# Kernel tuning notes

Measured on AMD Instinct MI355X. Metric: run time of the kernel, lower is better.

Reference implementation:

```python
import jax, jax.numpy as jnp
import numpy as np


def _gcn_conv(x, W, b, src, dst, num_nodes):
    # x: [N, F_in], W: [F_in, F_out], b: [F_out]
    # src/dst already include self-loops. Symmetric normalization per PyG GCNConv.
    ones = jnp.ones(src.shape[0], dtype=x.dtype)
    deg = jax.ops.segment_sum(ones, dst, num_segments=num_nodes)  # in-degree w/ self-loops
    dinv = jnp.where(deg > 0, jax.lax.rsqrt(deg), 0.0)
    norm = dinv[src] * dinv[dst]                                  # [E]
    h = x @ W                                                     # [N, F_out]
    msg = h[src] * norm[:, None]                                  # gather + scale
    out = jax.ops.segment_sum(msg, dst, num_segments=num_nodes)   # scatter-add
    return out + b


def setup_inputs() -> dict:
    key = jax.random.key(0)
    k1, k2, k3, k4, k5, k6 = jax.random.split(key, 6)
    N, E = 1000000, 4000000
    x = jax.random.normal(k1, (N, 4), dtype=jnp.float32)
    edge_index = jax.random.randint(k2, (2, E), 0, N, dtype=jnp.int64)
    W1 = jax.random.normal(k3, (4, 16), dtype=jnp.float32) * 0.5
    b1 = jax.random.normal(k4, (16,), dtype=jnp.float32) * 0.1
    W2 = jax.random.normal(k5, (16, 2), dtype=jnp.float32) * 0.25
    b2 = jax.random.normal(k6, (2,), dtype=jnp.float32) * 0.1
    return {"x": x, "edge_index": edge_index, "num_nodes": N,
            "W1": W1, "b1": b1, "W2": W2, "b2": b2}


def reference(x, edge_index, num_nodes, W1, b1, W2, b2):
    # Add self-loops once (GCNConv default add_self_loops=True)
    loop = jnp.arange(num_nodes, dtype=edge_index.dtype)
    src = jnp.concatenate([edge_index[0], loop])
    dst = jnp.concatenate([edge_index[1], loop])
    h = jax.nn.relu(_gcn_conv(x, W1, b1, src, dst, num_nodes))
    h = _gcn_conv(h, W2, b2, src, dst, num_nodes)
    return jax.nn.log_softmax(h, axis=1)
```

## Files before the change

kernel.cpp:

```cpp
#include <hip/hip_runtime.h>


typedef unsigned int u32;

#define BSHIFT 11
#define BNODES 2048
#define MAXBINS 1024
#define EPB 16384

__device__ __forceinline__ u32 pack_bf16(float a, float b) {
    u32 ua = __float_as_uint(a), ub = __float_as_uint(b);
    ua += 0x7FFFu + ((ua >> 16) & 1u);
    ub += 0x7FFFu + ((ub >> 16) & 1u);
    return (ua >> 16) | (ub & 0xFFFF0000u);
}
__device__ __forceinline__ float bf_lo(u32 p) { return __uint_as_float(p << 16); }
__device__ __forceinline__ float bf_hi(u32 p) { return __uint_as_float(p & 0xFFFF0000u); }

__global__ void k_bincount(const int* __restrict__ src, const int* __restrict__ dst,
                           int E, int NBINS, u32 HALF,
                           u32* __restrict__ binTotal, u32* __restrict__ bh) {
    __shared__ u32 h[MAXBINS];
    const int tid = threadIdx.x;
    for (int j = tid; j < MAXBINS; j += 256) h[j] = 0;
    __syncthreads();
    const int start = blockIdx.x * EPB;
    const int end = min(start + EPB, E);
    for (int e = start + tid; e < end; e += 256) {
        u32 d = (u32)dst[e];
        u32 b = ((d >> BSHIFT) << 1) | ((u32)src[e] >= HALF ? 1u : 0u);
        atomicAdd(&h[b], 1u);
    }
    __syncthreads();
    u32* bhrow = bh + (size_t)blockIdx.x * MAXBINS;
    for (int j = tid; j < NBINS; j += 256) {
        u32 c = h[j];
        bhrow[j] = c;
        if (c) atomicAdd(&binTotal[j], c);
    }
}

__global__ void k_binscan(const u32* __restrict__ binTotal,
                          u32* __restrict__ binBase,
                          u32* __restrict__ cursor, int NBINS, int E) {
    __shared__ u32 s[MAXBINS];
    const int tid = threadIdx.x;
    u32 v = (tid < NBINS) ? binTotal[tid] : 0u;
    s[tid] = v;
    __syncthreads();
    for (int d = 1; d < MAXBINS; d <<= 1) {
        u32 t = (tid >= d) ? s[tid - d] : 0u;
        __syncthreads();
        s[tid] += t;
        __syncthreads();
    }
    u32 excl = s[tid] - v;
    if (tid < NBINS) { binBase[tid] = excl; cursor[tid] = excl; }
    if (tid == 0) binBase[NBINS] = (u32)E;
}

__global__ void k_binscatter(const int* __restrict__ src, const int* __restrict__ dst,
                             int E, int NBINS, u32 HALF, u32* __restrict__ cursor,
                             const u32* __restrict__ bh, u32* __restrict__ rec) {
    __shared__ u32 h[MAXBINS];
    const int tid = threadIdx.x;
    const u32* bhrow = bh + (size_t)blockIdx.x * MAXBINS;
    for (int j = tid; j < MAXBINS; j += 256) h[j] = 0;
    __syncthreads();
    for (int j = tid; j < NBINS; j += 256) {
        u32 c = bhrow[j];
        if (c) h[j] = atomicAdd(&cursor[j], c);
    }
    __syncthreads();
    const int start = blockIdx.x * EPB;
    const int end = min(start + EPB, E);
    for (int e = start + tid; e < end; e += 256) {
        u32 d = (u32)dst[e];
        u32 sv = (u32)src[e];
        u32 b = ((d >> BSHIFT) << 1) | (sv >= HALF ? 1u : 0u);
        u32 slot = atomicAdd(&h[b], 1u);
        rec[slot] = sv | ((d & (BNODES - 1u)) << 20);
    }
}

__global__ void k_deg(const u32* __restrict__ rec, const u32* __restrict__ binBase,
                      const float4* __restrict__ x,
                      float* __restrict__ dinv, uint2* __restrict__ xd, int N) {
    __shared__ u32 deg[BNODES];
    const int tid = threadIdx.x;
    const int b = blockIdx.x;
    for (int j = tid; j < BNODES; j += 512) deg[j] = 0;
    __syncthreads();
    const u32 s0 = binBase[2 * b], s1 = binBase[2 * b + 2];
    for (u32 i = s0 + tid; i < s1; i += 512)
        atomicAdd(&deg[rec[i] >> 20], 1u);
    __syncthreads();
    const int nodeBase = b << BSHIFT;
    for (int n = tid; n < BNODES; n += 512) {
        int gn = nodeBase + n;
        if (gn < N) {
            float d = rsqrtf((float)(deg[n] + 1u));
            dinv[gn] = d;
            float4 xi = x[gn];
            xd[gn] = make_uint2(pack_bf16(xi.x * d, xi.y * d),
                                pack_bf16(xi.z * d, xi.w * d));
        }
    }
}

__global__ void k_l1(const u32* __restrict__ rec, const u32* __restrict__ binBase,
                     const float* __restrict__ dinv, const uint2* __restrict__ xd,
                     const float* __restrict__ W1, const float* __restrict__ b1,
                     const float* __restrict__ W2,
                     u32* __restrict__ h2, int N) {
    __shared__ float agg[BNODES * 4];
    const int tid = threadIdx.x;
    const int b = blockIdx.x;
    for (int j = tid; j < BNODES * 4; j += 1024) agg[j] = 0.f;
    __syncthreads();
    const u32 s0 = binBase[2 * b], s1 = binBase[2 * b + 2];

#define L1_EDGE(I) do {                                   \
        u32 r = rec[I];                                   \
        u32 s = r & 0xFFFFFu;                             \
        float* p = &agg[(r >> 20) * 4];                   \
        uint2 v = xd[s];                                  \
        atomicAdd(p + 0, bf_lo(v.x));                     \
        atomicAdd(p + 1, bf_hi(v.x));                     \
        atomicAdd(p + 2, bf_lo(v.y));                     \
        atomicAdd(p + 3, bf_hi(v.y));                     \
    } while (0)

    u32 i = s0 + tid;
    for (; i + 1024 < s1; i += 2048) { L1_EDGE(i); L1_EDGE(i + 1024); }
    if (i < s1) L1_EDGE(i);
#undef L1_EDGE
    __syncthreads();

    const int nodeBase = b << BSHIFT;
    for (int n = tid; n < BNODES; n += 1024) {
        int gn = nodeBase + n;
        if (gn >= N) continue;
        float di = dinv[gn];
        uint2 xs = xd[gn];
        float ax = (bf_lo(xs.x) + agg[n * 4 + 0]) * di;
        float ay = (bf_hi(xs.x) + agg[n * 4 + 1]) * di;
        float az = (bf_lo(xs.y) + agg[n * 4 + 2]) * di;
        float aw = (bf_hi(xs.y) + agg[n * 4 + 3]) * di;
        float g0 = 0.f, g1 = 0.f;
#pragma unroll
        for (int k = 0; k < 16; ++k) {
            float h = ax * W1[k] + ay * W1[16 + k] + az * W1[32 + k] + aw * W1[48 + k] + b1[k];
            h = fmaxf(h, 0.f);
            g0 += h * W2[2 * k];
            g1 += h * W2[2 * k + 1];
        }
        h2[gn] = pack_bf16(g0 * di, g1 * di);
    }
}

__global__ void k_l2(const u32* __restrict__ rec, const u32* __restrict__ binBase,
                     const float* __restrict__ dinv, const u32* __restrict__ h2,
                     const float* __restrict__ b2, float2* __restrict__ out, int N) {
    __shared__ float agg[BNODES * 2];
    const int tid = threadIdx.x;
    const int b = blockIdx.x;
    for (int j = tid; j < BNODES * 2; j += 1024) agg[j] = 0.f;
    __syncthreads();
    const u32 s0 = binBase[2 * b], s1 = binBase[2 * b + 2];

#define L2_EDGE(I) do {                                   \
        u32 r = rec[I];                                   \
        u32 s = r & 0xFFFFFu;                             \
        float* p = &agg[(r >> 20) * 2];                   \
        u32 v = h2[s];                                    \
        atomicAdd(p + 0, bf_lo(v));                       \
        atomicAdd(p + 1, bf_hi(v));                       \
    } while (0)

    u32 i = s0 + tid;
    for (; i + 1024 < s1; i += 2048) { L2_EDGE(i); L2_EDGE(i + 1024); }
    if (i < s1) L2_EDGE(i);
#undef L2_EDGE
    __syncthreads();

    const int nodeBase = b << BSHIFT;
    for (int n = tid; n < BNODES; n += 1024) {
        int gn = nodeBase + n;
        if (gn >= N) continue;
        float di = dinv[gn];
        u32 self = h2[gn];
        float g0 = (bf_lo(self) + agg[n * 2 + 0]) * di + b2[0];
        float g1 = (bf_hi(self) + agg[n * 2 + 1]) * di + b2[1];
        float m = fmaxf(g0, g1);
        float l = m + logf(expf(g0 - m) + expf(g1 - m));
        out[gn] = make_float2(g0 - l, g1 - l);
    }
}

extern "C" void kernel_launch(void* const* d_in, const int* in_sizes, int n_in,
                              void* d_out, int out_size, void* d_ws, size_t ws_size,
                              hipStream_t stream) {
    const float* x  = (const float*)d_in[0];
    const int*   ei = (const int*)d_in[1];
    const float* W1 = (const float*)d_in[3];
    const float* b1 = (const float*)d_in[4];
    const float* W2 = (const float*)d_in[5];
    const float* b2 = (const float*)d_in[6];

    const int N = in_sizes[0] / 4;
    const int E = in_sizes[1] / 2;
    const int* src = ei;
    const int* dst = ei + E;
    const int NB = (N + BNODES - 1) >> BSHIFT;
    const int NBINS = 2 * NB;
    const u32 HALF = (u32)(N >> 1);
    const int gA = (E + EPB - 1) / EPB;

    char* w = (char*)d_ws;
    u32*   rec  = (u32*)(w);
    float* dinv = (float*)(w + 4 * (size_t)E);
    uint2* xd   = (uint2*)(w + 4 * (size_t)E + 4 * (size_t)N);
    u32*   h2   = (u32*)(w + 4 * (size_t)E + 12 * (size_t)N);
    u32*   meta = (u32*)(w + 4 * (size_t)E + 16 * (size_t)N);
    u32*   binTotal = meta;
    u32*   binBase  = meta + MAXBINS;
    u32*   cursor   = meta + 2 * MAXBINS + 1;
    u32*   bh       = meta + 3 * MAXBINS + 2;

    hipMemsetAsync(binTotal, 0, sizeof(u32) * (size_t)NBINS, stream);
    k_bincount<<<gA, 256, 0, stream>>>(src, dst, E, NBINS, HALF, binTotal, bh);
    k_binscan<<<1, MAXBINS, 0, stream>>>(binTotal, binBase, cursor, NBINS, E);
    k_binscatter<<<gA, 256, 0, stream>>>(src, dst, E, NBINS, HALF, cursor, bh, rec);
    k_deg<<<NB, 512, 0, stream>>>(rec, binBase, (const float4*)x, dinv, xd, N);
    k_l1<<<NB, 1024, 0, stream>>>(rec, binBase, dinv, xd, W1, b1, W2, h2, N);
    k_l2<<<NB, 1024, 0, stream>>>(rec, binBase, dinv, h2, b2, (float2*)d_out, N);
}
```

Measured before the change: 313.4 us.

## Split edge bins by source quarter and batch gather loads in aggregation loops

Edges are now binned by destination block and by source quarter instead of source half, so each aggregation block walks its edges in four source-sorted groups. This is meant to give better cache locality on the random gathers of xd and h2. The scan kernel now handles two bins per thread to cover the doubled bin count. The layer-1 and layer-2 aggregation loops issue 4 or 8 independent index and gather loads before the shared-memory atomics, to raise memory-level parallelism. The cost is larger per-block histograms in the counting and scatter kernels and higher register use.

```diff
diff --git a/kernel.cpp b/kernel.cpp
--- a/kernel.cpp
+++ b/kernel.cpp
@@ -5,7 +5,7 @@
 
 #define BSHIFT 11
 #define BNODES 2048
-#define MAXBINS 1024
+#define MAXBINS 2048
 #define EPB 16384
 
 __device__ __forceinline__ u32 pack_bf16(float a, float b) {
@@ -17,8 +17,12 @@
 __device__ __forceinline__ float bf_lo(u32 p) { return __uint_as_float(p << 16); }
 __device__ __forceinline__ float bf_hi(u32 p) { return __uint_as_float(p & 0xFFFF0000u); }
 
+__device__ __forceinline__ u32 src_quarter(u32 sv, u32 Q1, u32 Q2, u32 Q3) {
+    return (sv >= Q2) ? ((sv >= Q3) ? 3u : 2u) : ((sv >= Q1) ? 1u : 0u);
+}
+
 __global__ void k_bincount(const int* __restrict__ src, const int* __restrict__ dst,
-                           int E, int NBINS, u32 HALF,
+                           int E, int NBINS, u32 Q1, u32 Q2, u32 Q3,
                            u32* __restrict__ binTotal, u32* __restrict__ bh) {
     __shared__ u32 h[MAXBINS];
     const int tid = threadIdx.x;
@@ -28,7 +32,7 @@
     const int end = min(start + EPB, E);
     for (int e = start + tid; e < end; e += 256) {
         u32 d = (u32)dst[e];
-        u32 b = ((d >> BSHIFT) << 1) | ((u32)src[e] >= HALF ? 1u : 0u);
+        u32 b = ((d >> BSHIFT) << 2) | src_quarter((u32)src[e], Q1, Q2, Q3);
         atomicAdd(&h[b], 1u);
     }
     __syncthreads();
@@ -43,24 +47,29 @@
 __global__ void k_binscan(const u32* __restrict__ binTotal,
                           u32* __restrict__ binBase,
                           u32* __restrict__ cursor, int NBINS, int E) {
-    __shared__ u32 s[MAXBINS];
-    const int tid = threadIdx.x;
-    u32 v = (tid < NBINS) ? binTotal[tid] : 0u;
-    s[tid] = v;
-    __syncthreads();
-    for (int d = 1; d < MAXBINS; d <<= 1) {
+    __shared__ u32 s[1024];
+    const int tid = threadIdx.x;
+    const int i0 = 2 * tid, i1 = 2 * tid + 1;
+    u32 v0 = (i0 < NBINS) ? binTotal[i0] : 0u;
+    u32 v1 = (i1 < NBINS) ? binTotal[i1] : 0u;
+    u32 p = v0 + v1;
+    s[tid] = p;
+    __syncthreads();
+    for (int d = 1; d < 1024; d <<= 1) {
         u32 t = (tid >= d) ? s[tid - d] : 0u;
         __syncthreads();
         s[tid] += t;
         __syncthreads();
     }
-    u32 excl = s[tid] - v;
-    if (tid < NBINS) { binBase[tid] = excl; cursor[tid] = excl; }
+    u32 excl = s[tid] - p;
+    if (i0 < NBINS) { binBase[i0] = excl;      cursor[i0] = excl; }
+    if (i1 < NBINS) { binBase[i1] = excl + v0; cursor[i1] = excl + v0; }
     if (tid == 0) binBase[NBINS] = (u32)E;
 }
 
 __global__ void k_binscatter(const int* __restrict__ src, const int* __restrict__ dst,
-                             int E, int NBINS, u32 HALF, u32* __restrict__ cursor,
+                             int E, int NBINS, u32 Q1, u32 Q2, u32 Q3,
+                             u32* __restrict__ cursor,
                              const u32* __restrict__ bh, u32* __restrict__ rec) {
     __shared__ u32 h[MAXBINS];
     const int tid = threadIdx.x;
@@ -77,7 +86,7 @@
     for (int e = start + tid; e < end; e += 256) {
         u32 d = (u32)dst[e];
         u32 sv = (u32)src[e];
-        u32 b = ((d >> BSHIFT) << 1) | (sv >= HALF ? 1u : 0u);
+        u32 b = ((d >> BSHIFT) << 2) | src_quarter(sv, Q1, Q2, Q3);
         u32 slot = atomicAdd(&h[b], 1u);
         rec[slot] = sv | ((d & (BNODES - 1u)) << 20);
     }
@@ -91,7 +100,7 @@
     const int b = blockIdx.x;
     for (int j = tid; j < BNODES; j += 512) deg[j] = 0;
     __syncthreads();
-    const u32 s0 = binBase[2 * b], s1 = binBase[2 * b + 2];
+    const u32 s0 = binBase[4 * b], s1 = binBase[4 * b + 4];
     for (u32 i = s0 + tid; i < s1; i += 512)
         atomicAdd(&deg[rec[i] >> 20], 1u);
     __syncthreads();
@@ -118,23 +127,32 @@
     const int b = blockIdx.x;
     for (int j = tid; j < BNODES * 4; j += 1024) agg[j] = 0.f;
     __syncthreads();
-    const u32 s0 = binBase[2 * b], s1 = binBase[2 * b + 2];
-
-#define L1_EDGE(I) do {                                   \
-        u32 r = rec[I];                                   \
-        u32 s = r & 0xFFFFFu;                             \
-        float* p = &agg[(r >> 20) * 4];                   \
-        uint2 v = xd[s];                                  \
-        atomicAdd(p + 0, bf_lo(v.x));                     \
-        atomicAdd(p + 1, bf_hi(v.x));                     \
-        atomicAdd(p + 2, bf_lo(v.y));                     \
-        atomicAdd(p + 3, bf_hi(v.y));                     \
+    const u32 s0 = binBase[4 * b], s1 = binBase[4 * b + 4];
+    const u32 T = 1024;
+
+#define L1_ACC(R, V) do {                                 \
+        float* p = &agg[((R) >> 20) * 4];                 \
+        atomicAdd(p + 0, bf_lo((V).x));                   \
+        atomicAdd(p + 1, bf_hi((V).x));                   \
+        atomicAdd(p + 2, bf_lo((V).y));                   \
+        atomicAdd(p + 3, bf_hi((V).y));                   \
     } while (0)
 
     u32 i = s0 + tid;
-    for (; i + 1024 < s1; i += 2048) { L1_EDGE(i); L1_EDGE(i + 1024); }
-    if (i < s1) L1_EDGE(i);
-#undef L1_EDGE
+    for (; i + 3 * T < s1; i += 4 * T) {
+        u32 r0 = rec[i], r1 = rec[i + T], r2 = rec[i + 2 * T], r3 = rec[i + 3 * T];
+        uint2 v0 = xd[r0 & 0xFFFFFu];
+        uint2 v1 = xd[r1 & 0xFFFFFu];
+        uint2 v2 = xd[r2 & 0xFFFFFu];
+        uint2 v3 = xd[r3 & 0xFFFFFu];
+        L1_ACC(r0, v0); L1_ACC(r1, v1); L1_ACC(r2, v2); L1_ACC(r3, v3);
+    }
+    for (; i < s1; i += T) {
+        u32 r = rec[i];
+        uint2 v = xd[r & 0xFFFFFu];
+        L1_ACC(r, v);
+    }
+#undef L1_ACC
     __syncthreads();
 
     const int nodeBase = b << BSHIFT;
@@ -167,21 +185,32 @@
     const int b = blockIdx.x;
     for (int j = tid; j < BNODES * 2; j += 1024) agg[j] = 0.f;
     __syncthreads();
-    const u32 s0 = binBase[2 * b], s1 = binBase[2 * b + 2];
-
-#define L2_EDGE(I) do {                                   \
-        u32 r = rec[I];                                   \
-        u32 s = r & 0xFFFFFu;                             \
-        float* p = &agg[(r >> 20) * 2];                   \
-        u32 v = h2[s];                                    \
-        atomicAdd(p + 0, bf_lo(v));                       \
-        atomicAdd(p + 1, bf_hi(v));                       \
+    const u32 s0 = binBase[4 * b], s1 = binBase[4 * b + 4];
+    const u32 T = 1024;
+
+#define L2_ACC(R, V) do {                                 \
+        float* p = &agg[((R) >> 20) * 2];                 \
+        atomicAdd(p + 0, bf_lo(V));                       \
+        atomicAdd(p + 1, bf_hi(V));                       \
     } while (0)
 
     u32 i = s0 + tid;
-    for (; i + 1024 < s1; i += 2048) { L2_EDGE(i); L2_EDGE(i + 1024); }
-    if (i < s1) L2_EDGE(i);
-#undef L2_EDGE
+    for (; i + 7 * T < s1; i += 8 * T) {
+        u32 r0 = rec[i],         r1 = rec[i + T],     r2 = rec[i + 2 * T], r3 = rec[i + 3 * T];
+        u32 r4 = rec[i + 4 * T], r5 = rec[i + 5 * T], r6 = rec[i + 6 * T], r7 = rec[i + 7 * T];
+        u32 v0 = h2[r0 & 0xFFFFFu], v1 = h2[r1 & 0xFFFFFu];
+        u32 v2 = h2[r2 & 0xFFFFFu], v3 = h2[r3 & 0xFFFFFu];
+        u32 v4 = h2[r4 & 0xFFFFFu], v5 = h2[r5 & 0xFFFFFu];
+        u32 v6 = h2[r6 & 0xFFFFFu], v7 = h2[r7 & 0xFFFFFu];
+        L2_ACC(r0, v0); L2_ACC(r1, v1); L2_ACC(r2, v2); L2_ACC(r3, v3);
+        L2_ACC(r4, v4); L2_ACC(r5, v5); L2_ACC(r6, v6); L2_ACC(r7, v7);
+    }
+    for (; i < s1; i += T) {
+        u32 r = rec[i];
+        u32 v = h2[r & 0xFFFFFu];
+        L2_ACC(r, v);
+    }
+#undef L2_ACC
     __syncthreads();
 
     const int nodeBase = b << BSHIFT;
@@ -213,8 +242,8 @@
     const int* src = ei;
     const int* dst = ei + E;
     const int NB = (N + BNODES - 1) >> BSHIFT;
-    const int NBINS = 2 * NB;
-    const u32 HALF = (u32)(N >> 1);
+    const int NBINS = 4 * NB;
+    const u32 Q1 = (u32)(N >> 2), Q2 = (u32)(N >> 1), Q3 = (u32)(3 * (N >> 2));
     const int gA = (E + EPB - 1) / EPB;
 
     char* w = (char*)d_ws;
@@ -229,9 +258,9 @@
     u32*   bh       = meta + 3 * MAXBINS + 2;
 
     hipMemsetAsync(binTotal, 0, sizeof(u32) * (size_t)NBINS, stream);
-    k_bincount<<<gA, 256, 0, stream>>>(src, dst, E, NBINS, HALF, binTotal, bh);
-    k_binscan<<<1, MAXBINS, 0, stream>>>(binTotal, binBase, cursor, NBINS, E);
-    k_binscatter<<<gA, 256, 0, stream>>>(src, dst, E, NBINS, HALF, cursor, bh, rec);
+    k_bincount<<<gA, 256, 0, stream>>>(src, dst, E, NBINS, Q1, Q2, Q3, binTotal, bh);
+    k_binscan<<<1, 1024, 0, stream>>>(binTotal, binBase, cursor, NBINS, E);
+    k_binscatter<<<gA, 256, 0, stream>>>(src, dst, E, NBINS, Q1, Q2, Q3, cursor, bh, rec);
     k_deg<<<NB, 512, 0, stream>>>(rec, binBase, (const float4*)x, dinv, xd, N);
     k_l1<<<NB, 1024, 0, stream>>>(rec, binBase, dinv, xd, W1, b1, W2, h2, N);
     k_l2<<<NB, 1024, 0, stream>>>(rec, binBase, dinv, h2, b2, (float2*)d_out, N);
```

Measured after the change: 323.8 us. 3.3% more time.
